# Optimization experiments

Measured on AMD Instinct MI355X. Metric: run time of the kernel, lower is better.

The kernel has to match this reference:

```python
import jax, jax.numpy as jnp
import numpy as np

S_DIM = 256   # summary_dim
L_DIM = 64    # latent_dim
H = 128       # hidden_dim
NL = 2        # num_layers
BATCH = 512
SEQ_LEN = 1024


def setup_inputs() -> dict:
    key = jax.random.key(0)
    ks = jax.random.split(key, 20)
    w = lambda k, shape, s=0.08: (jax.random.normal(k, shape, jnp.float32) * s)
    in0 = L_DIM + S_DIM  # LSTM layer-0 input size (cat of prev output + summary)
    return {
        "z_summary": jax.random.normal(ks[0], (BATCH, S_DIM), jnp.float32),
        "seq_len": SEQ_LEN,
        # summary -> initial hidden/cell states (Linear)
        "W_init_h": w(ks[1], (H * NL, S_DIM)),
        "b_init_h": w(ks[2], (H * NL,)),
        "W_init_c": w(ks[3], (H * NL, S_DIM)),
        "b_init_c": w(ks[4], (H * NL,)),
        # LSTM layer 0 (PyTorch gate order: i, f, g, o)
        "W_ih0": w(ks[5], (4 * H, in0)),
        "W_hh0": w(ks[6], (4 * H, H)),
        "b_ih0": w(ks[7], (4 * H,)),
        "b_hh0": w(ks[8], (4 * H,)),
        # LSTM layer 1
        "W_ih1": w(ks[9], (4 * H, H)),
        "W_hh1": w(ks[10], (4 * H, H)),
        "b_ih1": w(ks[11], (4 * H,)),
        "b_hh1": w(ks[12], (4 * H,)),
        # output head: Linear(H, L_DIM) + Tanh
        "W_out": w(ks[13], (L_DIM, H)),
        "b_out": w(ks[14], (L_DIM,)),
    }


def _lstm_cell(x, h, c, W_ih, W_hh, b_ih, b_hh):
    gates = x @ W_ih.T + b_ih + h @ W_hh.T + b_hh
    i, f, g, o = jnp.split(gates, 4, axis=-1)  # PyTorch gate order
    c_new = jax.nn.sigmoid(f) * c + jax.nn.sigmoid(i) * jnp.tanh(g)
    h_new = jax.nn.sigmoid(o) * jnp.tanh(c_new)
    return h_new, c_new


def reference(z_summary, seq_len, W_init_h, b_init_h, W_init_c, b_init_c,
              W_ih0, W_hh0, b_ih0, b_hh0, W_ih1, W_hh1, b_ih1, b_hh1,
              W_out, b_out):
    B = z_summary.shape[0]
    # init_hidden/init_cell: (B, NL*H) -> per-layer states (B, H)
    h0 = (z_summary @ W_init_h.T + b_init_h).reshape(B, NL, H)
    c0 = (z_summary @ W_init_c.T + b_init_c).reshape(B, NL, H)
    h_prev0 = jnp.zeros((B, L_DIM), z_summary.dtype)
    carry0 = (h0[:, 0], c0[:, 0], h0[:, 1], c0[:, 1], h_prev0)

    def step(carry, _):
        h_l0, c_l0, h_l1, c_l1, h_prev = carry
        x = jnp.concatenate([h_prev, z_summary], axis=-1)  # (B, L_DIM+S_DIM)
        h_l0, c_l0 = _lstm_cell(x, h_l0, c_l0, W_ih0, W_hh0, b_ih0, b_hh0)
        # dropout between layers is inference-mode identity
        h_l1, c_l1 = _lstm_cell(h_l0, h_l1, c_l1, W_ih1, W_hh1, b_ih1, b_hh1)
        h_t = jnp.tanh(h_l1 @ W_out.T + b_out)  # output head, fed back
        return (h_l0, c_l0, h_l1, c_l1, h_t), h_t

    _, ys = jax.lax.scan(step, carry0, None, length=seq_len)  # (T, B, L_DIM)
    return jnp.transpose(ys, (1, 0, 2))  # (B, T, L_DIM)
```

## Files before the change

kernel.cpp:

```cpp
#include <hip/hip_runtime.h>


#define DI __device__ __forceinline__

typedef float f32x4 __attribute__((ext_vector_type(4)));
typedef _Float16 h16x4 __attribute__((ext_vector_type(4)));
typedef _Float16 h16x8 __attribute__((ext_vector_type(8)));

DI float sigm_(float x) {
  float e = __expf(-x);
  return __builtin_amdgcn_rcpf(1.0f + e);
}
DI float tanh_(float x) {
  float e = __expf(-2.0f * x);
  return __builtin_fmaf(2.0f, __builtin_amdgcn_rcpf(1.0f + e), -1.0f);
}
DI h16x8 cvt8h(const float* __restrict__ p) {
  f32x4 a = *(const f32x4*)p;
  f32x4 b = *(const f32x4*)(p + 4);
  _Float16 t[8];
#pragma unroll
  for (int i = 0; i < 4; ++i) {
    t[i]     = (_Float16)a[i];
    t[4 + i] = (_Float16)b[i];
  }
  return *(h16x8*)t;
}

#define L_H0 0
#define L_H1 12800
#define L_WO 21504
#define L_AZ 37888
#define L_OB 46336
#define L_WL 48384
#define L_TOT 146688
static_assert(L_TOT <= 163840, "LDS budget (160 KiB/CU)");

template <int P>
DI void lstm_step(unsigned char* smem,
                  const h16x8 (&wf0)[20], const h16x8 (&wf1)[24],
                  float& c0r, float& c1r, h16x4 xzr, f32x4 bvr, float bo,
                  int a0off, int a1off, int v16, int wlb,
                  int w0off, int w1off, int oboff, int obro,
                  int col, int wv, int t, float* outp0) {
  constexpr int h0r = L_H0 + P * 6400, h0w = L_H0 + 6400 - P * 6400;
  constexpr int h1r = L_H1 + P * 4352, h1w = L_H1 + 4352 - P * 4352;

  f32x4 acc[4];
#pragma unroll
  for (int g = 0; g < 4; ++g) {
    float v = (float)xzr[g];
    f32x4 a = {v, v, v, v};
    acc[g] = a;
  }
#pragma unroll
  for (int kc = 0; kc < 6; ++kc) {
    h16x8 af = *(const h16x8*)(smem + h0r + a0off + kc * 64);
#pragma unroll
    for (int g = 0; g < 4; ++g) {
      h16x8 bf = (kc < 5)
          ? wf0[kc * 4 + g]
          : *(const h16x8*)(smem + wlb + g * 1024);
      acc[g] = __builtin_amdgcn_mfma_f32_16x16x32_f16(af, bf, acc[g], 0, 0, 0);
    }
  }
  {
    float ig = sigm_(acc[0][0]), fg = sigm_(acc[1][0]);
    float gg = tanh_(acc[2][0]), og = sigm_(acc[3][0]);
    c0r = fg * c0r + ig * gg;
    *(_Float16*)(smem + h0w + w0off) = (_Float16)(og * tanh_(c0r));
  }
  __syncthreads();

#pragma unroll
  for (int g = 0; g < 4; ++g) {
    f32x4 a = {bvr[g], bvr[g], bvr[g], bvr[g]};
    acc[g] = a;
  }
#pragma unroll
  for (int kc = 0; kc < 8; ++kc) {
    h16x8 af = (kc < 4)
        ? *(const h16x8*)(smem + h0w + a0off + kc * 64)
        : *(const h16x8*)(smem + h1r + a1off + (kc - 4) * 64);
#pragma unroll
    for (int g = 0; g < 4; ++g) {
      h16x8 bf = (kc < 6)
          ? wf1[kc * 4 + g]
          : *(const h16x8*)(smem + wlb + ((kc - 6) * 4 + g + 4) * 1024);
      acc[g] = __builtin_amdgcn_mfma_f32_16x16x32_f16(af, bf, acc[g], 0, 0, 0);
    }
  }
  {
    float ig = sigm_(acc[0][0]), fg = sigm_(acc[1][0]);
    float gg = tanh_(acc[2][0]), og = sigm_(acc[3][0]);
    c1r = fg * c1r + ig * gg;
    *(_Float16*)(smem + h1w + w1off) = (_Float16)(og * tanh_(c1r));
  }
  __syncthreads();

  if (wv < 4) {
    f32x4 ao = {bo, bo, bo, bo};
#pragma unroll
    for (int kc = 0; kc < 4; ++kc) {
      h16x8 af  = *(const h16x8*)(smem + h1w + a1off + kc * 64);
      h16x8 bfr = *(const h16x8*)(smem + L_WO + kc * 4096 + v16);
      ao = __builtin_amdgcn_mfma_f32_16x16x32_f16(af, bfr, ao, 0, 0, 0);
    }
    float v = tanh_(ao[0]);
    *(float*)(smem + L_OB + P * 1024 + oboff) = v;
    *(_Float16*)(smem + h0w + w0off + 256) = (_Float16)v;
  }
  __syncthreads();

  if (P) {
    float vv = *(const float*)(smem + L_OB + obro);
    *(outp0 + (unsigned)(t - 1) * 64u) = vv;
  }
}

__global__ __launch_bounds__(512, 2) void k_main(
    const float* __restrict__ z,
    const float* __restrict__ W_init_h, const float* __restrict__ b_init_h,
    const float* __restrict__ W_init_c, const float* __restrict__ b_init_c,
    const float* __restrict__ W_ih0, const float* __restrict__ W_hh0,
    const float* __restrict__ b_ih0, const float* __restrict__ b_hh0,
    const float* __restrict__ W_ih1, const float* __restrict__ W_hh1,
    const float* __restrict__ b_ih1, const float* __restrict__ b_hh1,
    const float* __restrict__ W_out, const float* __restrict__ b_out,
    float* __restrict__ out) {
  __shared__ __align__(16) unsigned char smem[L_TOT];
  const int tid = threadIdx.x;
  const int w = tid >> 6, l = tid & 63;
  const int l15 = l & 15, l4 = l >> 4;
  const int bl = blockIdx.x, b0i = bl << 2;
  const int col = 16 * w + l15;

  {
    int zm = tid >> 5, zk = (tid & 31) * 8;
    h16x8 zv;
    if ((zm & 3) == 0) {
      zv = cvt8h(z + (b0i + (zm >> 2)) * 256 + zk);
    } else {
      _Float16 t[8] = {};
      zv = *(h16x8*)t;
    }
    *(h16x8*)(smem + L_AZ + zm * 528 + zk * 2) = zv;
    for (int i = tid; i < 1024; i += 512) {
      int li = i & 63, f = i >> 6;
      int kc = f >> 2, wv = f & 3;
      int n = 16 * wv + (li & 15), k0 = kc * 32 + ((li >> 4) & 3) * 8;
      *(h16x8*)(smem + L_WO + i * 16) = cvt8h(W_out + n * 128 + k0);
    }
#pragma unroll
    for (int f = 0; f < 12; ++f) {
      int g = f & 3;
      int n = g * 128 + col;
      const float* src;
      if (f < 4) {
        src = W_ih0 + n * 320 + (32 + l4 * 8);
      } else {
        int kc = 6 + ((f - 4) >> 2);
        src = W_hh1 + n * 128 + (kc * 32 + l4 * 8 - 128);
      }
      *(h16x8*)(smem + L_WL + ((w * 12 + f) * 64 + l) * 16) = cvt8h(src);
    }
    if (tid < 256) {
      int r2 = tid >> 4, c2 = (tid & 15) * 4;
      h16x4 zz = {(_Float16)0, (_Float16)0, (_Float16)0, (_Float16)0};
      *(h16x4*)(smem + L_H0 + r2 * 400 + 256 + c2 * 2) = zz;
    }
  }
  f32x4 bvr;
#pragma unroll
  for (int g = 0; g < 4; ++g)
    bvr[g] = b_ih1[g * 128 + col] + b_hh1[g * 128 + col];
  float bo = (w < 4) ? b_out[col] : 0.0f;
  __syncthreads();

  float c0i, c1i;
  h16x4 xzr;
  {
    f32x4 xza[4], ha[2], ca[2];
#pragma unroll
    for (int g = 0; g < 4; ++g) {
      float b = b_ih0[g * 128 + col] + b_hh0[g * 128 + col];
      f32x4 a = {b, b, b, b}; xza[g] = a;
    }
#pragma unroll
    for (int layer = 0; layer < 2; ++layer) {
      float bh = b_init_h[layer * 128 + col];
      float bc = b_init_c[layer * 128 + col];
      f32x4 ah = {bh, bh, bh, bh}; ha[layer] = ah;
      f32x4 ac = {bc, bc, bc, bc}; ca[layer] = ac;
    }
#pragma unroll
    for (int kc = 0; kc < 8; ++kc) {
      h16x8 az = *(const h16x8*)(smem + L_AZ + l15 * 528 + kc * 64 + l4 * 16);
      int kofs = kc * 32 + l4 * 8;
#pragma unroll
      for (int g = 0; g < 4; ++g) {
        h16x8 bz = cvt8h(W_ih0 + (g * 128 + col) * 320 + 64 + kofs);
        xza[g] = __builtin_amdgcn_mfma_f32_16x16x32_f16(az, bz, xza[g], 0, 0, 0);
      }
#pragma unroll
      for (int layer = 0; layer < 2; ++layer) {
        h16x8 bh = cvt8h(W_init_h + (layer * 128 + col) * 256 + kofs);
        ha[layer] = __builtin_amdgcn_mfma_f32_16x16x32_f16(az, bh, ha[layer], 0, 0, 0);
        h16x8 bc = cvt8h(W_init_c + (layer * 128 + col) * 256 + kofs);
        ca[layer] = __builtin_amdgcn_mfma_f32_16x16x32_f16(az, bc, ca[layer], 0, 0, 0);
      }
    }
#pragma unroll
    for (int r = 0; r < 4; ++r) {
      int m = l4 * 4 + r;
      *(_Float16*)(smem + L_H0 + m * 400 + col * 2) = (_Float16)ha[0][r];
      *(_Float16*)(smem + L_H1 + m * 272 + col * 2) = (_Float16)ha[1][r];
    }
    c0i = ca[0][0]; c1i = ca[1][0];
    _Float16 t[4];
#pragma unroll
    for (int g = 0; g < 4; ++g) t[g] = (_Float16)xza[g][0];
    xzr = *(h16x4*)t;
  }

  h16x8 wf0[20], wf1[24];
#pragma unroll
  for (int kc = 0; kc < 5; ++kc)
#pragma unroll
    for (int g = 0; g < 4; ++g) {
      int n = g * 128 + col, k0 = kc * 32 + l4 * 8;
      const float* src = (k0 < 128) ? (W_hh0 + n * 128 + k0)
                                    : (W_ih0 + n * 320 + (k0 - 128));
      wf0[kc * 4 + g] = cvt8h(src);
    }
#pragma unroll
  for (int kc = 0; kc < 6; ++kc)
#pragma unroll
    for (int g = 0; g < 4; ++g) {
      int n = g * 128 + col, k0 = kc * 32 + l4 * 8;
      const float* src = (k0 < 128) ? (W_ih1 + n * 128 + k0)
                                    : (W_hh1 + n * 128 + (k0 - 128));
      wf1[kc * 4 + g] = cvt8h(src);
    }

  float c0r = c0i, c1r = c1i;

  const int a0off = (l15 & 12) * 400 + l4 * 16;
  const int a1off = (l15 & 12) * 272 + l4 * 16;
  const int v16   = tid * 16;
  const int wlb   = L_WL + (w * 12 * 64 + l) * 16;
  const int w0off = (4 * l4) * 400 + col * 2;
  const int w1off = (4 * l4) * 272 + col * 2;
  const int oboff = l4 * 256 + col * 4;
  const int obro  = (tid >> 8) * 1024 + ((tid >> 6) & 3) * 256 + (tid & 63) * 4;
  float* outp0 = out + (unsigned long long)(b0i + ((tid >> 6) & 3)) * 65536ull +
                 (tid >> 8) * 64 + (tid & 63);
  __syncthreads();

  for (int t2 = 0; t2 < 1024; t2 += 2) {
    lstm_step<0>(smem, wf0, wf1, c0r, c1r, xzr, bvr, bo, a0off, a1off, v16,
                 wlb, w0off, w1off, oboff, obro, col, w, t2, outp0);
    lstm_step<1>(smem, wf0, wf1, c0r, c1r, xzr, bvr, bo, a0off, a1off, v16,
                 wlb, w0off, w1off, oboff, obro, col, w, t2 + 1, outp0);
  }
}

extern "C" void kernel_launch(void* const* d_in, const int* in_sizes, int n_in,
                              void* d_out, int out_size, void* d_ws, size_t ws_size,
                              hipStream_t stream) {
  (void)in_sizes; (void)n_in; (void)out_size; (void)d_ws; (void)ws_size;
  const float* z        = (const float*)d_in[0];
  const float* W_init_h = (const float*)d_in[2];
  const float* b_init_h = (const float*)d_in[3];
  const float* W_init_c = (const float*)d_in[4];
  const float* b_init_c = (const float*)d_in[5];
  const float* W_ih0 = (const float*)d_in[6];
  const float* W_hh0 = (const float*)d_in[7];
  const float* b_ih0 = (const float*)d_in[8];
  const float* b_hh0 = (const float*)d_in[9];
  const float* W_ih1 = (const float*)d_in[10];
  const float* W_hh1 = (const float*)d_in[11];
  const float* b_ih1 = (const float*)d_in[12];
  const float* b_hh1 = (const float*)d_in[13];
  const float* W_out = (const float*)d_in[14];
  const float* b_out = (const float*)d_in[15];
  float* out = (float*)d_out;

  k_main<<<dim3(128), dim3(512), 0, stream>>>(
      z, W_init_h, b_init_h, W_init_c, b_init_c,
      W_ih0, W_hh0, b_ih0, b_hh0, W_ih1, W_hh1, b_ih1, b_hh1,
      W_out, b_out, out);
}
```

Measured before the change: 1.889 ms.

## Software-pipeline LSTM step: precompute next layer-0 h-part and layer-1 recurrent part early

Restructures the per-timestep schedule. The layer-0 gate MFMAs over the previous layer-0 hidden state for step t+1 are now issued at the end of step t, after the output head. The layer-1 MFMAs over its own previous hidden state are issued before the layer-0 nonlinearity and barrier. This moves more matrix work off the critical path between barriers so it can overlap with the dependent chain. In exchange it adds a carried accumulator across steps and raises register pressure.

```diff
diff --git a/kernel.cpp b/kernel.cpp
--- a/kernel.cpp
+++ b/kernel.cpp
@@ -6,6 +6,10 @@
 typedef float f32x4 __attribute__((ext_vector_type(4)));
 typedef _Float16 h16x4 __attribute__((ext_vector_type(4)));
 typedef _Float16 h16x8 __attribute__((ext_vector_type(8)));
+
+DI f32x4 mm(h16x8 a, h16x8 b, f32x4 c) {
+  return __builtin_amdgcn_mfma_f32_16x16x32_f16(a, b, c, 0, 0, 0);
+}
 
 DI float sigm_(float x) {
   float e = __expf(-x);
@@ -39,14 +43,78 @@
 template <int P>
 DI void lstm_step(unsigned char* smem,
                   const h16x8 (&wf0)[20], const h16x8 (&wf1)[24],
-                  float& c0r, float& c1r, h16x4 xzr, f32x4 bvr, float bo,
+                  f32x4 (&acc)[4], float& c0r, float& c1r,
+                  h16x4 xzr, f32x4 bvr, float bo,
                   int a0off, int a1off, int v16, int wlb,
                   int w0off, int w1off, int oboff, int obro,
-                  int col, int wv, int t, float* outp0) {
+                  int wv, int t, float* outp0) {
   constexpr int h0r = L_H0 + P * 6400, h0w = L_H0 + 6400 - P * 6400;
   constexpr int h1r = L_H1 + P * 4352, h1w = L_H1 + 4352 - P * 4352;
 
-  f32x4 acc[4];
+  f32x4 acc2[4];
+  {
+    h16x8 af4 = *(const h16x8*)(smem + h0r + a0off + 4 * 64);
+    h16x8 af5 = *(const h16x8*)(smem + h0r + a0off + 5 * 64);
+#pragma unroll
+    for (int g = 0; g < 4; ++g)
+      acc[g] = mm(af4, wf0[16 + g], acc[g]);
+#pragma unroll
+    for (int g = 0; g < 4; ++g) {
+      h16x8 bf = *(const h16x8*)(smem + wlb + g * 1024);
+      acc[g] = mm(af5, bf, acc[g]);
+    }
+  }
+#pragma unroll
+  for (int g = 0; g < 4; ++g) {
+    f32x4 a = {bvr[g], bvr[g], bvr[g], bvr[g]};
+    acc2[g] = a;
+  }
+#pragma unroll
+  for (int kc = 4; kc < 8; ++kc) {
+    h16x8 af = *(const h16x8*)(smem + h1r + a1off + (kc - 4) * 64);
+#pragma unroll
+    for (int g = 0; g < 4; ++g) {
+      h16x8 bf = (kc < 6)
+          ? wf1[kc * 4 + g]
+          : *(const h16x8*)(smem + wlb + ((kc - 6) * 4 + g + 4) * 1024);
+      acc2[g] = mm(af, bf, acc2[g]);
+    }
+  }
+  {
+    float ig = sigm_(acc[0][0]), fg = sigm_(acc[1][0]);
+    float gg = tanh_(acc[2][0]), og = sigm_(acc[3][0]);
+    c0r = fg * c0r + ig * gg;
+    *(_Float16*)(smem + h0w + w0off) = (_Float16)(og * tanh_(c0r));
+  }
+  __syncthreads();
+
+#pragma unroll
+  for (int kc = 0; kc < 4; ++kc) {
+    h16x8 af = *(const h16x8*)(smem + h0w + a0off + kc * 64);
+#pragma unroll
+    for (int g = 0; g < 4; ++g)
+      acc2[g] = mm(af, wf1[kc * 4 + g], acc2[g]);
+  }
+  {
+    float ig = sigm_(acc2[0][0]), fg = sigm_(acc2[1][0]);
+    float gg = tanh_(acc2[2][0]), og = sigm_(acc2[3][0]);
+    c1r = fg * c1r + ig * gg;
+    *(_Float16*)(smem + h1w + w1off) = (_Float16)(og * tanh_(c1r));
+  }
+  __syncthreads();
+
+  if (wv < 4) {
+    f32x4 ao = {bo, bo, bo, bo};
+#pragma unroll
+    for (int kc = 0; kc < 4; ++kc) {
+      h16x8 af  = *(const h16x8*)(smem + h1w + a1off + kc * 64);
+      h16x8 bfr = *(const h16x8*)(smem + L_WO + kc * 4096 + v16);
+      ao = mm(af, bfr, ao);
+    }
+    float v = tanh_(ao[0]);
+    *(float*)(smem + L_OB + P * 1024 + oboff) = v;
+    *(_Float16*)(smem + h0w + w0off + 256) = (_Float16)v;
+  }
 #pragma unroll
   for (int g = 0; g < 4; ++g) {
     float v = (float)xzr[g];
@@ -54,61 +122,11 @@
     acc[g] = a;
   }
 #pragma unroll
-  for (int kc = 0; kc < 6; ++kc) {
-    h16x8 af = *(const h16x8*)(smem + h0r + a0off + kc * 64);
-#pragma unroll
-    for (int g = 0; g < 4; ++g) {
-      h16x8 bf = (kc < 5)
-          ? wf0[kc * 4 + g]
-          : *(const h16x8*)(smem + wlb + g * 1024);
-      acc[g] = __builtin_amdgcn_mfma_f32_16x16x32_f16(af, bf, acc[g], 0, 0, 0);
-    }
-  }
-  {
-    float ig = sigm_(acc[0][0]), fg = sigm_(acc[1][0]);
-    float gg = tanh_(acc[2][0]), og = sigm_(acc[3][0]);
-    c0r = fg * c0r + ig * gg;
-    *(_Float16*)(smem + h0w + w0off) = (_Float16)(og * tanh_(c0r));
-  }
-  __syncthreads();
-
-#pragma unroll
-  for (int g = 0; g < 4; ++g) {
-    f32x4 a = {bvr[g], bvr[g], bvr[g], bvr[g]};
-    acc[g] = a;
-  }
-#pragma unroll
-  for (int kc = 0; kc < 8; ++kc) {
-    h16x8 af = (kc < 4)
-        ? *(const h16x8*)(smem + h0w + a0off + kc * 64)
-        : *(const h16x8*)(smem + h1r + a1off + (kc - 4) * 64);
-#pragma unroll
-    for (int g = 0; g < 4; ++g) {
-      h16x8 bf = (kc < 6)
-          ? wf1[kc * 4 + g]
-          : *(const h16x8*)(smem + wlb + ((kc - 6) * 4 + g + 4) * 1024);
-      acc[g] = __builtin_amdgcn_mfma_f32_16x16x32_f16(af, bf, acc[g], 0, 0, 0);
-    }
-  }
-  {
-    float ig = sigm_(acc[0][0]), fg = sigm_(acc[1][0]);
-    float gg = tanh_(acc[2][0]), og = sigm_(acc[3][0]);
-    c1r = fg * c1r + ig * gg;
-    *(_Float16*)(smem + h1w + w1off) = (_Float16)(og * tanh_(c1r));
-  }
-  __syncthreads();
-
-  if (wv < 4) {
-    f32x4 ao = {bo, bo, bo, bo};
-#pragma unroll
-    for (int kc = 0; kc < 4; ++kc) {
-      h16x8 af  = *(const h16x8*)(smem + h1w + a1off + kc * 64);
-      h16x8 bfr = *(const h16x8*)(smem + L_WO + kc * 4096 + v16);
-      ao = __builtin_amdgcn_mfma_f32_16x16x32_f16(af, bfr, ao, 0, 0, 0);
-    }
-    float v = tanh_(ao[0]);
-    *(float*)(smem + L_OB + P * 1024 + oboff) = v;
-    *(_Float16*)(smem + h0w + w0off + 256) = (_Float16)v;
+  for (int kc = 0; kc < 4; ++kc) {
+    h16x8 af = *(const h16x8*)(smem + h0w + a0off + kc * 64);
+#pragma unroll
+    for (int g = 0; g < 4; ++g)
+      acc[g] = mm(af, wf0[kc * 4 + g], acc[g]);
   }
   __syncthreads();
 
@@ -200,14 +218,14 @@
 #pragma unroll
       for (int g = 0; g < 4; ++g) {
         h16x8 bz = cvt8h(W_ih0 + (g * 128 + col) * 320 + 64 + kofs);
-        xza[g] = __builtin_amdgcn_mfma_f32_16x16x32_f16(az, bz, xza[g], 0, 0, 0);
+        xza[g] = mm(az, bz, xza[g]);
       }
 #pragma unroll
       for (int layer = 0; layer < 2; ++layer) {
         h16x8 bh = cvt8h(W_init_h + (layer * 128 + col) * 256 + kofs);
-        ha[layer] = __builtin_amdgcn_mfma_f32_16x16x32_f16(az, bh, ha[layer], 0, 0, 0);
+        ha[layer] = mm(az, bh, ha[layer]);
         h16x8 bc = cvt8h(W_init_c + (layer * 128 + col) * 256 + kofs);
-        ca[layer] = __builtin_amdgcn_mfma_f32_16x16x32_f16(az, bc, ca[layer], 0, 0, 0);
+        ca[layer] = mm(az, bc, ca[layer]);
       }
     }
 #pragma unroll
@@ -257,11 +275,26 @@
                  (tid >> 8) * 64 + (tid & 63);
   __syncthreads();
 
+  f32x4 acc[4];
+#pragma unroll
+  for (int g = 0; g < 4; ++g) {
+    float v = (float)xzr[g];
+    f32x4 a = {v, v, v, v};
+    acc[g] = a;
+  }
+#pragma unroll
+  for (int kc = 0; kc < 4; ++kc) {
+    h16x8 af = *(const h16x8*)(smem + L_H0 + a0off + kc * 64);
+#pragma unroll
+    for (int g = 0; g < 4; ++g)
+      acc[g] = mm(af, wf0[kc * 4 + g], acc[g]);
+  }
+
   for (int t2 = 0; t2 < 1024; t2 += 2) {
-    lstm_step<0>(smem, wf0, wf1, c0r, c1r, xzr, bvr, bo, a0off, a1off, v16,
-                 wlb, w0off, w1off, oboff, obro, col, w, t2, outp0);
-    lstm_step<1>(smem, wf0, wf1, c0r, c1r, xzr, bvr, bo, a0off, a1off, v16,
-                 wlb, w0off, w1off, oboff, obro, col, w, t2 + 1, outp0);
+    lstm_step<0>(smem, wf0, wf1, acc, c0r, c1r, xzr, bvr, bo, a0off, a1off,
+                 v16, wlb, w0off, w1off, oboff, obro, w, t2, outp0);
+    lstm_step<1>(smem, wf0, wf1, acc, c0r, c1r, xzr, bvr, bo, a0off, a1off,
+                 v16, wlb, w0off, w1off, oboff, obro, w, t2 + 1, outp0);
   }
 }
 
```

Measured after the change: 2.062 ms. 1.09x slower.
